# Performance work log

Hardware: AMD Instinct MI355X
Metric: run time of the kernel (lower is better)

Reference implementation:

```python
import jax, jax.numpy as jnp
import numpy as np

BETA = 0.1


def setup_inputs() -> dict:
    key = jax.random.key(0)
    ks = jax.random.split(key, 8)
    B, S, H, V = 4, 512, 2048, 32000
    return {
        "lin_weight": jax.random.normal(ks[0], (V, H), jnp.float32) * 0.02,
        "_input": jax.random.normal(ks[1], (B, S, H), jnp.float32),
        "attention_mask": jnp.ones((B, S), jnp.float32),
        "rewards": jax.random.normal(ks[2], (B,), jnp.float32),
        "bias": jax.random.normal(ks[3], (V,), jnp.float32) * 0.02,
        "ref_input": jax.random.normal(ks[4], (B, S, H), jnp.float32),
        "ref_weight": jax.random.normal(ks[5], (V, H), jnp.float32) * 0.02,
        "ref_bias": jax.random.normal(ks[6], (V,), jnp.float32) * 0.02,
    }


def _seq_logps(x, w, b, mask):
    # logits: [B,S,V]; per-token max log-softmax, masked, summed over seq
    logits = jnp.einsum("bsh,vh->bsv", x, w) + b
    lp = jax.nn.log_softmax(logits, axis=-1)
    seq = (jnp.max(lp, axis=-1) * mask).sum(axis=-1)  # [B]
    return logits, seq


def reference(lin_weight, _input, attention_mask, rewards, bias, ref_input, ref_weight, ref_bias):
    policy_logits, seq_log_probs = _seq_logps(_input, lin_weight, bias, attention_mask)
    _, ref_seq_logps = _seq_logps(ref_input, ref_weight, ref_bias, attention_mask)
    ref_seq_logps = jax.lax.stop_gradient(ref_seq_logps)

    adv = rewards - rewards.mean()
    std = jnp.std(rewards, ddof=1)  # torch unbiased std
    adv = jnp.where(std > 0, adv / std, adv)

    kl_div = seq_log_probs - ref_seq_logps
    loss = (-(adv * seq_log_probs) + BETA * kl_div).mean()

    metrics = (
        seq_log_probs.mean(),
        jnp.std(seq_log_probs, ddof=1),
        policy_logits.mean(),
        kl_div.mean(),
    )
    return (loss,) + metrics
```

## Files before the change

### kernel.cpp

```cpp
#include <hip/hip_runtime.h>
#include <hip/hip_fp16.h>
#include <math.h>

#define TOK 2048
#define HD 2048
#define VOC 32000
#define BM 256
#define BN 256
#define BK 64
#define NT (HD/BK)
#define NCH (VOC/64)
#define NBLK ((TOK/BM)*(VOC/BN))

typedef _Float16 half8 __attribute__((ext_vector_type(8)));
typedef float float4v __attribute__((ext_vector_type(4)));

#define GLB __attribute__((address_space(1)))
#define LDSAS __attribute__((address_space(3)))

static __device__ __forceinline__ void gload_lds16(const void* g, void* l) {
  __builtin_amdgcn_global_load_lds((const GLB unsigned int*)g,
                                   (LDSAS unsigned int*)l, 16, 0, 0);
}

static __device__ __forceinline__ float4v mfma16(half8 a, half8 b, float4v c) {
  return __builtin_amdgcn_mfma_f32_16x16x32_f16(a, b, c, 0, 0, 0);
}

__global__ void cvt_f32_f16(const float* __restrict__ in,
                            _Float16* __restrict__ out, int n8) {
  for (int i = blockIdx.x * blockDim.x + threadIdx.x; i < n8;
       i += gridDim.x * blockDim.x) {
    float4v a = *(const float4v*)(in + (size_t)i*8);
    float4v b = *(const float4v*)(in + (size_t)i*8 + 4);
    half8 h;
    #pragma unroll
    for (int j=0;j<4;j++) { h[j] = (_Float16)a[j]; h[4+j] = (_Float16)b[j]; }
    *(half8*)(out + (size_t)i*8) = h;
  }
}

template<int CB, bool SG1, bool SG2, int VMN>
__device__ __forceinline__ void ktile(
    unsigned char* ldsby, const char* Xb, const char* Wb,
    int sA0, int sA1, int sB0, int sB1, int ldst0, int ldst1, int kbn,
    const int (&aofs)[8], const int (&bofs)[4], float4v (&acc)[8][4])
{
  constexpr int U0 = CB, U1 = CB + 16384, U2 = CB + 32768, U3 = CB + 49152;
  half8 af1[8], bf1[4], af2lo[4], bf2[4], af2hi[4];

  #pragma unroll
  for (int n=0;n<4;n++) bf1[n] = *(const half8*)(ldsby + U1 + bofs[n]);
  #pragma unroll
  for (int m=0;m<8;m++) af1[m] = *(const half8*)(ldsby + U0 + aofs[m]);
  if (SG1) {
    gload_lds16(Xb + (sA0 + kbn + 64), ldsby + ((CB^65536) + 32768) + ldst0);
    gload_lds16(Xb + (sA1 + kbn + 64), ldsby + ((CB^65536) + 32768) + ldst1);
    gload_lds16(Wb + (sB0 + kbn + 64), ldsby + ((CB^65536) + 49152) + ldst0);
    gload_lds16(Wb + (sB1 + kbn + 64), ldsby + ((CB^65536) + 49152) + ldst1);
  }
  __builtin_amdgcn_s_setprio(1);
  #pragma unroll
  for (int m=0;m<4;m++)
    #pragma unroll
    for (int n=0;n<4;n++)
      acc[m][n] = mfma16(af1[m], bf1[n], acc[m][n]);
  #pragma unroll
  for (int n=0;n<4;n++) bf2[n]   = *(const half8*)(ldsby + U3 + bofs[n]);
  #pragma unroll
  for (int m=0;m<4;m++) af2lo[m] = *(const half8*)(ldsby + U2 + aofs[m]);
  #pragma unroll
  for (int m=4;m<8;m++)
    #pragma unroll
    for (int n=0;n<4;n++)
      acc[m][n] = mfma16(af1[m], bf1[n], acc[m][n]);
  __builtin_amdgcn_s_setprio(0);
  __builtin_amdgcn_s_barrier();

  #pragma unroll
  for (int m=0;m<4;m++) af2hi[m] = *(const half8*)(ldsby + U2 + aofs[4+m]);
  if (SG2) {
    gload_lds16(Xb + (sA0 + kbn + 128), ldsby + (CB + 0)     + ldst0);
    gload_lds16(Xb + (sA1 + kbn + 128), ldsby + (CB + 0)     + ldst1);
    gload_lds16(Wb + (sB0 + kbn + 128), ldsby + (CB + 16384) + ldst0);
    gload_lds16(Wb + (sB1 + kbn + 128), ldsby + (CB + 16384) + ldst1);
  }
  __builtin_amdgcn_s_setprio(1);
  #pragma unroll
  for (int m=0;m<4;m++)
    #pragma unroll
    for (int n=0;n<4;n++)
      acc[m][n] = mfma16(af2lo[m], bf2[n], acc[m][n]);
  #pragma unroll
  for (int m=0;m<4;m++)
    #pragma unroll
    for (int n=0;n<4;n++)
      acc[4+m][n] = mfma16(af2hi[m], bf2[n], acc[4+m][n]);
  __builtin_amdgcn_s_setprio(0);
  if (VMN == 4)      asm volatile("s_waitcnt vmcnt(4)" ::: "memory");
  else if (VMN == 0) asm volatile("s_waitcnt vmcnt(0)" ::: "memory");
  __builtin_amdgcn_s_barrier();
}

__global__ __launch_bounds__(512, 2) void gemm_stats_f16(
    const _Float16* __restrict__ Xh, const _Float16* __restrict__ Wh,
    const float* __restrict__ bias,
    float* __restrict__ pmax, float* __restrict__ psum,
    float* __restrict__ bsum, int computeSum)
{
  __shared__ unsigned char ldsbuf[131072];
  unsigned char* ldsby = ldsbuf;

  int bid = blockIdx.x;
  int swz = (bid & 7) * (NBLK/8) + (bid >> 3);
  int rowt = swz & 7;
  int colt = swz >> 3;
  int brow = rowt * BM;
  int bcol = colt * BN;

  int tid  = threadIdx.x;
  int lane = tid & 63;
  int wv   = tid >> 6;
  int wr   = wv >> 2;
  int wc   = wv & 3;
  int l15  = lane & 15;
  int q    = lane >> 4;

  int aswz = (((((l15 & 1) << 2) | q) ^ ((l15 >> 1) & 7)) << 4) + ((l15 >> 1) << 7);
  int aofs[8], bofs[4];
  #pragma unroll
  for (int m = 0; m < 8; m++) aofs[m] = wr*8192 + m*1024 + aswz;
  #pragma unroll
  for (int n = 0; n < 4; n++) bofs[n] = wc*4096 + n*1024 + aswz;

  int s8  = (tid & 7) ^ ((tid >> 3) & 7);
  int rl  = wv*16 + (((tid >> 3) & 7) << 1) + (s8 >> 2);
  int kc  = (s8 & 3) << 4;
  int sA0 = (brow + rl)*(HD*2) + kc;
  int sA1 = sA0 + 128*(HD*2);
  int sB0 = (bcol + rl)*(HD*2) + kc;
  int sB1 = sB0 + 128*(HD*2);
  int ldst0 = (wv << 10);
  int ldst1 = (wv << 10) + 8192;

  const char* Xb = (const char*)Xh;
  const char* Wb = (const char*)Wh;

  float4v acc[8][4];
  #pragma unroll
  for (int m=0;m<8;m++)
    #pragma unroll
    for (int n=0;n<4;n++) acc[m][n] = (float4v){0.f,0.f,0.f,0.f};

  gload_lds16(Xb + sA0,       ldsby + 0     + ldst0);
  gload_lds16(Xb + sA1,       ldsby + 0     + ldst1);
  gload_lds16(Wb + sB0,       ldsby + 16384 + ldst0);
  gload_lds16(Wb + sB1,       ldsby + 16384 + ldst1);
  gload_lds16(Xb + (sA0+64),  ldsby + 32768 + ldst0);
  gload_lds16(Xb + (sA1+64),  ldsby + 32768 + ldst1);
  gload_lds16(Wb + (sB0+64),  ldsby + 49152 + ldst0);
  gload_lds16(Wb + (sB1+64),  ldsby + 49152 + ldst1);
  gload_lds16(Xb + (sA0+128), ldsby + 65536 + ldst0);
  gload_lds16(Xb + (sA1+128), ldsby + 65536 + ldst1);
  gload_lds16(Wb + (sB0+128), ldsby + 81920 + ldst0);
  gload_lds16(Wb + (sB1+128), ldsby + 81920 + ldst1);
  asm volatile("s_waitcnt vmcnt(4)" ::: "memory");
  __builtin_amdgcn_s_barrier();

  int kbn = 128;
  #pragma unroll 1
  for (int i = 0; i < 15; ++i) {
    ktile<0,     true, true, 4>(ldsby, Xb, Wb, sA0,sA1,sB0,sB1, ldst0,ldst1, kbn, aofs, bofs, acc);
    kbn += 128;
    ktile<65536, true, true, 4>(ldsby, Xb, Wb, sA0,sA1,sB0,sB1, ldst0,ldst1, kbn, aofs, bofs, acc);
    kbn += 128;
  }
  ktile<0,     true,  false, 0>(ldsby, Xb, Wb, sA0,sA1,sB0,sB1, ldst0,ldst1, kbn, aofs, bofs, acc);
  kbn += 128;
  ktile<65536, false, false, -1>(ldsby, Xb, Wb, sA0,sA1,sB0,sB1, ldst0,ldst1, kbn, aofs, bofs, acc);

  float bv[4];
  #pragma unroll
  for (int n=0;n<4;n++) bv[n] = bias[bcol + wc*64 + n*16 + l15];

  float lsum = 0.f;
  int ch = colt*4 + wc;
  #pragma unroll
  for (int m=0;m<8;m++) {
    #pragma unroll
    for (int r=0;r<4;r++) {
      float v0 = acc[m][0][r] + bv[0];
      float v1 = acc[m][1][r] + bv[1];
      float v2 = acc[m][2][r] + bv[2];
      float v3 = acc[m][3][r] + bv[3];
      if (computeSum) lsum += v0+v1+v2+v3;
      float mx = fmaxf(fmaxf(v0,v1), fmaxf(v2,v3));
      #pragma unroll
      for (int off=1; off<16; off<<=1) mx = fmaxf(mx, __shfl_xor(mx, off, 64));
      float se = __expf(v0-mx)+__expf(v1-mx)+__expf(v2-mx)+__expf(v3-mx);
      #pragma unroll
      for (int off=1; off<16; off<<=1) se += __shfl_xor(se, off, 64);
      if (l15 == 0) {
        int row = brow + wr*128 + m*16 + (lane>>4)*4 + r;
        pmax[(size_t)row*NCH + ch] = mx;
        psum[(size_t)row*NCH + ch] = se;
      }
    }
  }

  if (computeSum) {
    #pragma unroll
    for (int off=1; off<64; off<<=1) lsum += __shfl_xor(lsum, off, 64);
    __syncthreads();
    float* red = (float*)ldsbuf;
    if (lane == 0) red[wv] = lsum;
    __syncthreads();
    if (tid == 0) {
      float s = 0.f;
      for (int w=0; w<8; w++) s += red[w];
      bsum[blockIdx.x] = s;
    }
  }
}

__global__ void row_combine(const float* __restrict__ pmax,
                            const float* __restrict__ psum,
                            const float* __restrict__ mask,
                            float* __restrict__ tok)
{
  int row = blockIdx.x;
  int lane = threadIdx.x;
  float M = -INFINITY;
  for (int c = lane; c < NCH; c += 64) M = fmaxf(M, pmax[(size_t)row*NCH + c]);
  #pragma unroll
  for (int off=1; off<64; off<<=1) M = fmaxf(M, __shfl_xor(M, off, 64));
  float L = 0.f;
  for (int c = lane; c < NCH; c += 64)
    L += psum[(size_t)row*NCH + c] * __expf(pmax[(size_t)row*NCH + c] - M);
  #pragma unroll
  for (int off=1; off<64; off<<=1) L += __shfl_xor(L, off, 64);
  if (lane == 0) tok[row] = -logf(L) * mask[row];
}

__global__ void finalize(const float* __restrict__ tokP,
                         const float* __restrict__ tokR,
                         const float* __restrict__ rewards,
                         const float* __restrict__ bsum, int nbsum,
                         float* __restrict__ out)
{
  __shared__ float red[256];
  __shared__ float seqP[4], seqR[4];
  int t = threadIdx.x;
  for (int b=0; b<4; b++) {
    float v = tokP[b*512 + t] + tokP[b*512 + 256 + t];
    red[t] = v; __syncthreads();
    for (int s=128; s>0; s>>=1) { if (t < s) red[t] += red[t+s]; __syncthreads(); }
    if (t == 0) seqP[b] = red[0];
    __syncthreads();
    v = tokR[b*512 + t] + tokR[b*512 + 256 + t];
    red[t] = v; __syncthreads();
    for (int s=128; s>0; s>>=1) { if (t < s) red[t] += red[t+s]; __syncthreads(); }
    if (t == 0) seqR[b] = red[0];
    __syncthreads();
  }
  float ls = 0.f;
  for (int i=t; i<nbsum; i+=256) ls += bsum[i];
  red[t] = ls; __syncthreads();
  for (int s=128; s>0; s>>=1) { if (t < s) red[t] += red[t+s]; __syncthreads(); }
  if (t == 0) {
    float r0=rewards[0], r1=rewards[1], r2=rewards[2], r3=rewards[3];
    float rm = (r0+r1+r2+r3)*0.25f;
    float var = ((r0-rm)*(r0-rm)+(r1-rm)*(r1-rm)+(r2-rm)*(r2-rm)+(r3-rm)*(r3-rm))/3.f;
    float rstd = sqrtf(var);
    float adv[4] = {r0-rm, r1-rm, r2-rm, r3-rm};
    if (rstd > 0.f) { for (int b=0;b<4;b++) adv[b] /= rstd; }
    float loss=0.f, sm=0.f, km=0.f;
    for (int b=0;b<4;b++) {
      float kl = seqP[b] - seqR[b];
      loss += -(adv[b]*seqP[b]) + 0.1f*kl;
      sm += seqP[b]; km += kl;
    }
    loss *= 0.25f; sm *= 0.25f; km *= 0.25f;
    float sv = 0.f;
    for (int b=0;b<4;b++) { float d = seqP[b]-sm; sv += d*d; }
    float sstd = sqrtf(sv/3.f);
    out[0] = loss;
    out[1] = sm;
    out[2] = sstd;
    out[3] = red[0] / ((float)TOK * (float)VOC);
    out[4] = km;
  }
}

extern "C" void kernel_launch(void* const* d_in, const int* in_sizes, int n_in,
                              void* d_out, int out_size, void* d_ws, size_t ws_size,
                              hipStream_t stream) {
  const float* W    = (const float*)d_in[0];
  const float* X    = (const float*)d_in[1];
  const float* mask = (const float*)d_in[2];
  const float* rew  = (const float*)d_in[3];
  const float* bias = (const float*)d_in[4];
  const float* Xr   = (const float*)d_in[5];
  const float* Wr   = (const float*)d_in[6];
  const float* br   = (const float*)d_in[7];
  float* out = (float*)d_out;

  float* pmax = (float*)d_ws;
  float* psum = pmax + (size_t)TOK*NCH;
  float* tokP = psum + (size_t)TOK*NCH;
  float* tokR = tokP + TOK;
  float* bsum = tokR + TOK;

  size_t headFloats = (size_t)TOK*NCH*2 + TOK*2 + 4096;
  size_t offXh = headFloats * 4;
  _Float16* Xh = (_Float16*)((unsigned char*)d_ws + offXh);
  _Float16* Wh = (_Float16*)((unsigned char*)d_ws + offXh + (size_t)TOK*HD*2);

  cvt_f32_f16<<<2048, 256, 0, stream>>>(X,  Xh, TOK*HD/8);
  cvt_f32_f16<<<2048, 256, 0, stream>>>(W,  Wh, VOC*HD/8);
  gemm_stats_f16<<<NBLK, 512, 0, stream>>>(Xh, Wh, bias, pmax, psum, bsum, 1);
  row_combine<<<TOK, 64, 0, stream>>>(pmax, psum, mask, tokP);
  cvt_f32_f16<<<2048, 256, 0, stream>>>(Xr, Xh, TOK*HD/8);
  cvt_f32_f16<<<2048, 256, 0, stream>>>(Wr, Wh, VOC*HD/8);
  gemm_stats_f16<<<NBLK, 512, 0, stream>>>(Xh, Wh, br, pmax, psum, bsum, 0);
  row_combine<<<TOK, 64, 0, stream>>>(pmax, psum, mask, tokR);
  finalize<<<1, 256, 0, stream>>>(tokP, tokR, rew, bsum, NBLK, out);
}
```

Measured before the change: 678.5 us.

## Load fp32 weights directly into registers and convert in-kernel, dropping W conversion pass

Removes the separate fp32-to-fp16 conversion kernels for the 32000x2048 weight matrices. The GEMM now reads fp32 W straight from global memory into per-lane registers with a one-step register prefetch, then packs it to fp16 with cvt_pkrtz before the MFMAs. Only the X tile is staged through LDS, so LDS shrinks to 64KB. This removes a full read and write of each weight matrix, but each block reads the weights at twice the bytes from global memory without LDS sharing. It also adds register pressure and uses round-toward-zero conversion.

Result: slower. 1.361 ms (+100.6%).

```diff
diff --git a/kernel.cpp b/kernel.cpp
--- a/kernel.cpp
+++ b/kernel.cpp
@@ -13,6 +13,8 @@
 #define NBLK ((TOK/BM)*(VOC/BN))
 
 typedef _Float16 half8 __attribute__((ext_vector_type(8)));
+typedef _Float16 half2v __attribute__((ext_vector_type(2)));
+typedef __fp16   fp16x2 __attribute__((ext_vector_type(2)));
 typedef float float4v __attribute__((ext_vector_type(4)));
 
 #define GLB __attribute__((address_space(1)))
@@ -25,6 +27,17 @@
 
 static __device__ __forceinline__ float4v mfma16(half8 a, half8 b, float4v c) {
   return __builtin_amdgcn_mfma_f32_16x16x32_f16(a, b, c, 0, 0, 0);
+}
+
+static __device__ __forceinline__ half8 cvt8(float4v a, float4v b) {
+  half2v p0 = __builtin_bit_cast(half2v, __builtin_amdgcn_cvt_pkrtz(a[0], a[1]));
+  half2v p1 = __builtin_bit_cast(half2v, __builtin_amdgcn_cvt_pkrtz(a[2], a[3]));
+  half2v p2 = __builtin_bit_cast(half2v, __builtin_amdgcn_cvt_pkrtz(b[0], b[1]));
+  half2v p3 = __builtin_bit_cast(half2v, __builtin_amdgcn_cvt_pkrtz(b[2], b[3]));
+  half8 h;
+  h[0]=p0[0]; h[1]=p0[1]; h[2]=p1[0]; h[3]=p1[1];
+  h[4]=p2[0]; h[5]=p2[1]; h[6]=p3[0]; h[7]=p3[1];
+  return h;
 }
 
 __global__ void cvt_f32_f16(const float* __restrict__ in,
@@ -40,75 +53,69 @@
   }
 }
 
-template<int CB, bool SG1, bool SG2, int VMN>
+template<int CB, bool SGA1, bool SGA2, bool SGB2>
 __device__ __forceinline__ void ktile(
-    unsigned char* ldsby, const char* Xb, const char* Wb,
-    int sA0, int sA1, int sB0, int sB1, int ldst0, int ldst1, int kbn,
-    const int (&aofs)[8], const int (&bofs)[4], float4v (&acc)[8][4])
+    unsigned char* ldsby, const char* Xb,
+    const char* const (&wb)[4], int koffA,
+    int sA0, int sA1, int ldst0, int ldst1, int kbn,
+    const int (&aofs)[8], float4v (&bstg)[4][2], float4v (&acc)[8][4])
 {
-  constexpr int U0 = CB, U1 = CB + 16384, U2 = CB + 32768, U3 = CB + 49152;
-  half8 af1[8], bf1[4], af2lo[4], bf2[4], af2hi[4];
-
-  #pragma unroll
-  for (int n=0;n<4;n++) bf1[n] = *(const half8*)(ldsby + U1 + bofs[n]);
-  #pragma unroll
-  for (int m=0;m<8;m++) af1[m] = *(const half8*)(ldsby + U0 + aofs[m]);
-  if (SG1) {
-    gload_lds16(Xb + (sA0 + kbn + 64), ldsby + ((CB^65536) + 32768) + ldst0);
-    gload_lds16(Xb + (sA1 + kbn + 64), ldsby + ((CB^65536) + 32768) + ldst1);
-    gload_lds16(Wb + (sB0 + kbn + 64), ldsby + ((CB^65536) + 49152) + ldst0);
-    gload_lds16(Wb + (sB1 + kbn + 64), ldsby + ((CB^65536) + 49152) + ldst1);
+  half8 af[8], bf[4];
+
+  if (SGA1) {
+    gload_lds16(Xb + (sA0 + kbn + 64), ldsby + ((CB^32768) + 16384) + ldst0);
+    gload_lds16(Xb + (sA1 + kbn + 64), ldsby + ((CB^32768) + 16384) + ldst1);
+  }
+  #pragma unroll
+  for (int m=0;m<8;m++) af[m] = *(const half8*)(ldsby + CB + aofs[m]);
+  #pragma unroll
+  for (int n=0;n<4;n++) bf[n] = cvt8(bstg[n][0], bstg[n][1]);
+  #pragma unroll
+  for (int n=0;n<4;n++) {
+    bstg[n][0] = *(const float4v*)(wb[n] + koffA);
+    bstg[n][1] = *(const float4v*)(wb[n] + koffA + 16);
   }
   __builtin_amdgcn_s_setprio(1);
   #pragma unroll
-  for (int m=0;m<4;m++)
+  for (int m=0;m<8;m++)
     #pragma unroll
     for (int n=0;n<4;n++)
-      acc[m][n] = mfma16(af1[m], bf1[n], acc[m][n]);
-  #pragma unroll
-  for (int n=0;n<4;n++) bf2[n]   = *(const half8*)(ldsby + U3 + bofs[n]);
-  #pragma unroll
-  for (int m=0;m<4;m++) af2lo[m] = *(const half8*)(ldsby + U2 + aofs[m]);
-  #pragma unroll
-  for (int m=4;m<8;m++)
-    #pragma unroll
-    for (int n=0;n<4;n++)
-      acc[m][n] = mfma16(af1[m], bf1[n], acc[m][n]);
+      acc[m][n] = mfma16(af[m], bf[n], acc[m][n]);
   __builtin_amdgcn_s_setprio(0);
   __builtin_amdgcn_s_barrier();
 
-  #pragma unroll
-  for (int m=0;m<4;m++) af2hi[m] = *(const half8*)(ldsby + U2 + aofs[4+m]);
-  if (SG2) {
-    gload_lds16(Xb + (sA0 + kbn + 128), ldsby + (CB + 0)     + ldst0);
-    gload_lds16(Xb + (sA1 + kbn + 128), ldsby + (CB + 0)     + ldst1);
-    gload_lds16(Wb + (sB0 + kbn + 128), ldsby + (CB + 16384) + ldst0);
-    gload_lds16(Wb + (sB1 + kbn + 128), ldsby + (CB + 16384) + ldst1);
+  if (SGA2) {
+    gload_lds16(Xb + (sA0 + kbn + 128), ldsby + CB + ldst0);
+    gload_lds16(Xb + (sA1 + kbn + 128), ldsby + CB + ldst1);
+  }
+  #pragma unroll
+  for (int m=0;m<8;m++) af[m] = *(const half8*)(ldsby + CB + 16384 + aofs[m]);
+  #pragma unroll
+  for (int n=0;n<4;n++) bf[n] = cvt8(bstg[n][0], bstg[n][1]);
+  if (SGB2) {
+    #pragma unroll
+    for (int n=0;n<4;n++) {
+      bstg[n][0] = *(const float4v*)(wb[n] + koffA + 128);
+      bstg[n][1] = *(const float4v*)(wb[n] + koffA + 144);
+    }
   }
   __builtin_amdgcn_s_setprio(1);
   #pragma unroll
-  for (int m=0;m<4;m++)
+  for (int m=0;m<8;m++)
     #pragma unroll
     for (int n=0;n<4;n++)
-      acc[m][n] = mfma16(af2lo[m], bf2[n], acc[m][n]);
-  #pragma unroll
-  for (int m=0;m<4;m++)
-    #pragma unroll
-    for (int n=0;n<4;n++)
-      acc[4+m][n] = mfma16(af2hi[m], bf2[n], acc[4+m][n]);
+      acc[m][n] = mfma16(af[m], bf[n], acc[m][n]);
   __builtin_amdgcn_s_setprio(0);
-  if (VMN == 4)      asm volatile("s_waitcnt vmcnt(4)" ::: "memory");
-  else if (VMN == 0) asm volatile("s_waitcnt vmcnt(0)" ::: "memory");
   __builtin_amdgcn_s_barrier();
 }
 
 __global__ __launch_bounds__(512, 2) void gemm_stats_f16(
-    const _Float16* __restrict__ Xh, const _Float16* __restrict__ Wh,
+    const _Float16* __restrict__ Xh, const float* __restrict__ W32,
     const float* __restrict__ bias,
     float* __restrict__ pmax, float* __restrict__ psum,
     float* __restrict__ bsum, int computeSum)
 {
-  __shared__ unsigned char ldsbuf[131072];
+  __shared__ unsigned char ldsbuf[65536];
   unsigned char* ldsby = ldsbuf;
 
   int bid = blockIdx.x;
@@ -127,24 +134,28 @@
   int q    = lane >> 4;
 
   int aswz = (((((l15 & 1) << 2) | q) ^ ((l15 >> 1) & 7)) << 4) + ((l15 >> 1) << 7);
-  int aofs[8], bofs[4];
+  int aofs[8];
   #pragma unroll
   for (int m = 0; m < 8; m++) aofs[m] = wr*8192 + m*1024 + aswz;
-  #pragma unroll
-  for (int n = 0; n < 4; n++) bofs[n] = wc*4096 + n*1024 + aswz;
 
   int s8  = (tid & 7) ^ ((tid >> 3) & 7);
   int rl  = wv*16 + (((tid >> 3) & 7) << 1) + (s8 >> 2);
   int kc  = (s8 & 3) << 4;
   int sA0 = (brow + rl)*(HD*2) + kc;
   int sA1 = sA0 + 128*(HD*2);
-  int sB0 = (bcol + rl)*(HD*2) + kc;
-  int sB1 = sB0 + 128*(HD*2);
   int ldst0 = (wv << 10);
   int ldst1 = (wv << 10) + 8192;
 
   const char* Xb = (const char*)Xh;
-  const char* Wb = (const char*)Wh;
+
+  const char* wb[4];
+  {
+    const char* Wc = (const char*)W32;
+    int v0 = bcol + wc*64 + l15;
+    #pragma unroll
+    for (int n=0;n<4;n++)
+      wb[n] = Wc + (size_t)(v0 + n*16) * (HD*4) + q*32;
+  }
 
   float4v acc[8][4];
   #pragma unroll
@@ -152,32 +163,34 @@
     #pragma unroll
     for (int n=0;n<4;n++) acc[m][n] = (float4v){0.f,0.f,0.f,0.f};
 
+  float4v bstg[4][2];
+
+  #pragma unroll
+  for (int n=0;n<4;n++) {
+    bstg[n][0] = *(const float4v*)(wb[n] + 0);
+    bstg[n][1] = *(const float4v*)(wb[n] + 16);
+  }
   gload_lds16(Xb + sA0,       ldsby + 0     + ldst0);
   gload_lds16(Xb + sA1,       ldsby + 0     + ldst1);
-  gload_lds16(Wb + sB0,       ldsby + 16384 + ldst0);
-  gload_lds16(Wb + sB1,       ldsby + 16384 + ldst1);
-  gload_lds16(Xb + (sA0+64),  ldsby + 32768 + ldst0);
-  gload_lds16(Xb + (sA1+64),  ldsby + 32768 + ldst1);
-  gload_lds16(Wb + (sB0+64),  ldsby + 49152 + ldst0);
-  gload_lds16(Wb + (sB1+64),  ldsby + 49152 + ldst1);
-  gload_lds16(Xb + (sA0+128), ldsby + 65536 + ldst0);
-  gload_lds16(Xb + (sA1+128), ldsby + 65536 + ldst1);
-  gload_lds16(Wb + (sB0+128), ldsby + 81920 + ldst0);
-  gload_lds16(Wb + (sB1+128), ldsby + 81920 + ldst1);
-  asm volatile("s_waitcnt vmcnt(4)" ::: "memory");
+  gload_lds16(Xb + (sA0+64),  ldsby + 16384 + ldst0);
+  gload_lds16(Xb + (sA1+64),  ldsby + 16384 + ldst1);
+  gload_lds16(Xb + (sA0+128), ldsby + 32768 + ldst0);
+  gload_lds16(Xb + (sA1+128), ldsby + 32768 + ldst1);
+  asm volatile("s_waitcnt vmcnt(0)" ::: "memory");
   __builtin_amdgcn_s_barrier();
 
-  int kbn = 128;
+  int kbn   = 128;
+  int koffA = 128;
   #pragma unroll 1
   for (int i = 0; i < 15; ++i) {
-    ktile<0,     true, true, 4>(ldsby, Xb, Wb, sA0,sA1,sB0,sB1, ldst0,ldst1, kbn, aofs, bofs, acc);
-    kbn += 128;
-    ktile<65536, true, true, 4>(ldsby, Xb, Wb, sA0,sA1,sB0,sB1, ldst0,ldst1, kbn, aofs, bofs, acc);
-    kbn += 128;
-  }
-  ktile<0,     true,  false, 0>(ldsby, Xb, Wb, sA0,sA1,sB0,sB1, ldst0,ldst1, kbn, aofs, bofs, acc);
-  kbn += 128;
-  ktile<65536, false, false, -1>(ldsby, Xb, Wb, sA0,sA1,sB0,sB1, ldst0,ldst1, kbn, aofs, bofs, acc);
+    ktile<0,     true, true, true>(ldsby, Xb, wb, koffA, sA0,sA1, ldst0,ldst1, kbn, aofs, bstg, acc);
+    kbn += 128; koffA += 256;
+    ktile<32768, true, true, true>(ldsby, Xb, wb, koffA, sA0,sA1, ldst0,ldst1, kbn, aofs, bstg, acc);
+    kbn += 128; koffA += 256;
+  }
+  ktile<0,     true,  false, true >(ldsby, Xb, wb, koffA, sA0,sA1, ldst0,ldst1, kbn, aofs, bstg, acc);
+  kbn += 128; koffA += 256;
+  ktile<32768, false, false, false>(ldsby, Xb, wb, koffA, sA0,sA1, ldst0,ldst1, kbn, aofs, bstg, acc);
 
   float bv[4];
   #pragma unroll
@@ -314,15 +327,12 @@
   size_t headFloats = (size_t)TOK*NCH*2 + TOK*2 + 4096;
   size_t offXh = headFloats * 4;
   _Float16* Xh = (_Float16*)((unsigned char*)d_ws + offXh);
-  _Float16* Wh = (_Float16*)((unsigned char*)d_ws + offXh + (size_t)TOK*HD*2);
 
   cvt_f32_f16<<<2048, 256, 0, stream>>>(X,  Xh, TOK*HD/8);
-  cvt_f32_f16<<<2048, 256, 0, stream>>>(W,  Wh, VOC*HD/8);
-  gemm_stats_f16<<<NBLK, 512, 0, stream>>>(Xh, Wh, bias, pmax, psum, bsum, 1);
+  gemm_stats_f16<<<NBLK, 512, 0, stream>>>(Xh, W, bias, pmax, psum, bsum, 1);
   row_combine<<<TOK, 64, 0, stream>>>(pmax, psum, mask, tokP);
   cvt_f32_f16<<<2048, 256, 0, stream>>>(Xr, Xh, TOK*HD/8);
-  cvt_f32_f16<<<2048, 256, 0, stream>>>(Wr, Wh, VOC*HD/8);
-  gemm_stats_f16<<<NBLK, 512, 0, stream>>>(Xh, Wh, br, pmax, psum, bsum, 0);
+  gemm_stats_f16<<<NBLK, 512, 0, stream>>>(Xh, Wr, br, pmax, psum, bsum, 0);
   row_combine<<<TOK, 64, 0, stream>>>(pmax, psum, mask, tokR);
   finalize<<<1, 256, 0, stream>>>(tokP, tokR, rew, bsum, NBLK, out);
 }
```

## Prefetch next K-tile LDS fragments across tile boundary in GEMM main loop

Applied to the files above, without the earlier changes.

Restructures the GEMM inner pipeline so the first A/B fragments of the next K-tile are read from LDS during the previous tile's MFMA tail and carried in registers (pfa/pfb). This hides LDS read latency at the start of each tile. A vmcnt wait is added before the mid-tile barrier so the prefetched buffer is ready. The cost is more live VGPRs under a 512x2 launch bound, which risks spills or reduced occupancy, plus an extra wait point that may stall global loads.

After: 679.5 us. Within noise of the previous version (+0.2%).

```diff
diff --git a/kernel.cpp b/kernel.cpp
--- a/kernel.cpp
+++ b/kernel.cpp
@@ -40,19 +40,18 @@
   }
 }
 
-template<int CB, bool SG1, bool SG2, int VMN>
+template<int CB, bool SG1, bool SG2, bool PF, int VM1, int VM2>
 __device__ __forceinline__ void ktile(
     unsigned char* ldsby, const char* Xb, const char* Wb,
-    int sA0, int sA1, int sB0, int sB1, int ldst0, int ldst1, int kbn,
-    const int (&aofs)[8], const int (&bofs)[4], float4v (&acc)[8][4])
+    int sA0, int sA1, int sB0, int sB1,
+    int ldst0, int ldst1, int kbn,
+    const int (&aofs)[8], const int (&bofs)[4],
+    half8 (&pfa)[4], half8 (&pfb)[4], float4v (&acc)[8][4])
 {
-  constexpr int U0 = CB, U1 = CB + 16384, U2 = CB + 32768, U3 = CB + 49152;
-  half8 af1[8], bf1[4], af2lo[4], bf2[4], af2hi[4];
-
-  #pragma unroll
-  for (int n=0;n<4;n++) bf1[n] = *(const half8*)(ldsby + U1 + bofs[n]);
-  #pragma unroll
-  for (int m=0;m<8;m++) af1[m] = *(const half8*)(ldsby + U0 + aofs[m]);
+  half8 hi[4], qalo[4], qb[4];
+
+  #pragma unroll
+  for (int m=0;m<4;m++) hi[m] = *(const half8*)(ldsby + CB + aofs[4+m]);
   if (SG1) {
     gload_lds16(Xb + (sA0 + kbn + 64), ldsby + ((CB^65536) + 32768) + ldst0);
     gload_lds16(Xb + (sA1 + kbn + 64), ldsby + ((CB^65536) + 32768) + ldst1);
@@ -64,24 +63,26 @@
   for (int m=0;m<4;m++)
     #pragma unroll
     for (int n=0;n<4;n++)
-      acc[m][n] = mfma16(af1[m], bf1[n], acc[m][n]);
-  #pragma unroll
-  for (int n=0;n<4;n++) bf2[n]   = *(const half8*)(ldsby + U3 + bofs[n]);
-  #pragma unroll
-  for (int m=0;m<4;m++) af2lo[m] = *(const half8*)(ldsby + U2 + aofs[m]);
-  #pragma unroll
-  for (int m=4;m<8;m++)
+      acc[m][n] = mfma16(pfa[m], pfb[n], acc[m][n]);
+  #pragma unroll
+  for (int n=0;n<4;n++) qb[n]   = *(const half8*)(ldsby + CB + 49152 + bofs[n]);
+  #pragma unroll
+  for (int m=0;m<4;m++) qalo[m] = *(const half8*)(ldsby + CB + 32768 + aofs[m]);
+  #pragma unroll
+  for (int m=0;m<4;m++)
     #pragma unroll
     for (int n=0;n<4;n++)
-      acc[m][n] = mfma16(af1[m], bf1[n], acc[m][n]);
+      acc[4+m][n] = mfma16(hi[m], pfb[n], acc[4+m][n]);
   __builtin_amdgcn_s_setprio(0);
+  if (VM1==4)      asm volatile("s_waitcnt vmcnt(4)" ::: "memory");
+  else if (VM1==0) asm volatile("s_waitcnt vmcnt(0)" ::: "memory");
   __builtin_amdgcn_s_barrier();
 
   #pragma unroll
-  for (int m=0;m<4;m++) af2hi[m] = *(const half8*)(ldsby + U2 + aofs[4+m]);
+  for (int m=0;m<4;m++) hi[m] = *(const half8*)(ldsby + CB + 32768 + aofs[4+m]);
   if (SG2) {
-    gload_lds16(Xb + (sA0 + kbn + 128), ldsby + (CB + 0)     + ldst0);
-    gload_lds16(Xb + (sA1 + kbn + 128), ldsby + (CB + 0)     + ldst1);
+    gload_lds16(Xb + (sA0 + kbn + 128), ldsby + CB + ldst0);
+    gload_lds16(Xb + (sA1 + kbn + 128), ldsby + CB + ldst1);
     gload_lds16(Wb + (sB0 + kbn + 128), ldsby + (CB + 16384) + ldst0);
     gload_lds16(Wb + (sB1 + kbn + 128), ldsby + (CB + 16384) + ldst1);
   }
@@ -90,15 +91,21 @@
   for (int m=0;m<4;m++)
     #pragma unroll
     for (int n=0;n<4;n++)
-      acc[m][n] = mfma16(af2lo[m], bf2[n], acc[m][n]);
+      acc[m][n] = mfma16(qalo[m], qb[n], acc[m][n]);
+  if (PF) {
+    #pragma unroll
+    for (int n=0;n<4;n++) pfb[n] = *(const half8*)(ldsby + (CB^65536) + 16384 + bofs[n]);
+    #pragma unroll
+    for (int m=0;m<4;m++) pfa[m] = *(const half8*)(ldsby + (CB^65536) + aofs[m]);
+  }
   #pragma unroll
   for (int m=0;m<4;m++)
     #pragma unroll
     for (int n=0;n<4;n++)
-      acc[4+m][n] = mfma16(af2hi[m], bf2[n], acc[4+m][n]);
+      acc[4+m][n] = mfma16(hi[m], qb[n], acc[4+m][n]);
   __builtin_amdgcn_s_setprio(0);
-  if (VMN == 4)      asm volatile("s_waitcnt vmcnt(4)" ::: "memory");
-  else if (VMN == 0) asm volatile("s_waitcnt vmcnt(0)" ::: "memory");
+  if (VM2==4)      asm volatile("s_waitcnt vmcnt(4)" ::: "memory");
+  else if (VM2==0) asm volatile("s_waitcnt vmcnt(0)" ::: "memory");
   __builtin_amdgcn_s_barrier();
 }
 
@@ -167,17 +174,23 @@
   asm volatile("s_waitcnt vmcnt(4)" ::: "memory");
   __builtin_amdgcn_s_barrier();
 
+  half8 pfa[4], pfb[4];
+  #pragma unroll
+  for (int n=0;n<4;n++) pfb[n] = *(const half8*)(ldsby + 16384 + bofs[n]);
+  #pragma unroll
+  for (int m=0;m<4;m++) pfa[m] = *(const half8*)(ldsby + aofs[m]);
+
   int kbn = 128;
   #pragma unroll 1
   for (int i = 0; i < 15; ++i) {
-    ktile<0,     true, true, 4>(ldsby, Xb, Wb, sA0,sA1,sB0,sB1, ldst0,ldst1, kbn, aofs, bofs, acc);
+    ktile<0,     true,true,true, 4,4>(ldsby, Xb, Wb, sA0,sA1,sB0,sB1, ldst0,ldst1, kbn, aofs, bofs, pfa, pfb, acc);
     kbn += 128;
-    ktile<65536, true, true, 4>(ldsby, Xb, Wb, sA0,sA1,sB0,sB1, ldst0,ldst1, kbn, aofs, bofs, acc);
+    ktile<65536, true,true,true, 4,4>(ldsby, Xb, Wb, sA0,sA1,sB0,sB1, ldst0,ldst1, kbn, aofs, bofs, pfa, pfb, acc);
     kbn += 128;
   }
-  ktile<0,     true,  false, 0>(ldsby, Xb, Wb, sA0,sA1,sB0,sB1, ldst0,ldst1, kbn, aofs, bofs, acc);
+  ktile<0,     true,false,true, 4,0>(ldsby, Xb, Wb, sA0,sA1,sB0,sB1, ldst0,ldst1, kbn, aofs, bofs, pfa, pfb, acc);
   kbn += 128;
-  ktile<65536, false, false, -1>(ldsby, Xb, Wb, sA0,sA1,sB0,sB1, ldst0,ldst1, kbn, aofs, bofs, acc);
+  ktile<65536, false,false,false, -1,-1>(ldsby, Xb, Wb, sA0,sA1,sB0,sB1, ldst0,ldst1, kbn, aofs, bofs, pfa, pfb, acc);
 
   float bv[4];
   #pragma unroll
```

## Restructure GEMM k-tile into four barrier-separated phases with smaller fragment sets

Applied to the files above, without the earlier changes.

Splits each double k-step into four phases, each loading 4 A and 4 B fragments from LDS and issuing 16 MFMAs. Global-to-LDS prefetches are spread across the phases, and every phase ends with a barrier plus an lgkmcnt wait. This cuts live fragment registers and interleaves loads with compute in a ping-pong style across the two waves per SIMD. The cost is more barriers and sched_barriers, which may serialize work and lose overlap.

Result: no change. 692.0 us (+2.0%).

```diff
diff --git a/kernel.cpp b/kernel.cpp
--- a/kernel.cpp
+++ b/kernel.cpp
@@ -40,62 +40,88 @@
   }
 }
 
-template<int CB, bool SG1, bool SG2, int VMN>
+template<int CB, bool SG01, bool SG23, int VMN>
 __device__ __forceinline__ void ktile(
     unsigned char* ldsby, const char* Xb, const char* Wb,
-    int sA0, int sA1, int sB0, int sB1, int ldst0, int ldst1, int kbn,
+    int sA0, int sA1, int sB0, int sB1,
+    int ldst0, int ldst1, int kbn,
     const int (&aofs)[8], const int (&bofs)[4], float4v (&acc)[8][4])
 {
-  constexpr int U0 = CB, U1 = CB + 16384, U2 = CB + 32768, U3 = CB + 49152;
-  half8 af1[8], bf1[4], af2lo[4], bf2[4], af2hi[4];
-
-  #pragma unroll
-  for (int n=0;n<4;n++) bf1[n] = *(const half8*)(ldsby + U1 + bofs[n]);
-  #pragma unroll
-  for (int m=0;m<8;m++) af1[m] = *(const half8*)(ldsby + U0 + aofs[m]);
-  if (SG1) {
+  half8 af[4], bf[4];
+
+  #pragma unroll
+  for (int m=0;m<4;m++) af[m] = *(const half8*)(ldsby + CB + aofs[m]);
+  #pragma unroll
+  for (int n=0;n<4;n++) bf[n] = *(const half8*)(ldsby + CB + 16384 + bofs[n]);
+  if (SG01) {
     gload_lds16(Xb + (sA0 + kbn + 64), ldsby + ((CB^65536) + 32768) + ldst0);
     gload_lds16(Xb + (sA1 + kbn + 64), ldsby + ((CB^65536) + 32768) + ldst1);
+  }
+  __builtin_amdgcn_s_barrier();
+  asm volatile("s_waitcnt lgkmcnt(0)" ::: "memory");
+  __builtin_amdgcn_sched_barrier(0);
+  __builtin_amdgcn_s_setprio(1);
+  #pragma unroll
+  for (int m=0;m<4;m++)
+    #pragma unroll
+    for (int n=0;n<4;n++)
+      acc[m][n] = mfma16(af[m], bf[n], acc[m][n]);
+  __builtin_amdgcn_s_setprio(0);
+  __builtin_amdgcn_s_barrier();
+
+  #pragma unroll
+  for (int m=0;m<4;m++) af[m] = *(const half8*)(ldsby + CB + aofs[4+m]);
+  if (SG01) {
     gload_lds16(Wb + (sB0 + kbn + 64), ldsby + ((CB^65536) + 49152) + ldst0);
     gload_lds16(Wb + (sB1 + kbn + 64), ldsby + ((CB^65536) + 49152) + ldst1);
   }
+  __builtin_amdgcn_s_barrier();
+  asm volatile("s_waitcnt lgkmcnt(0)" ::: "memory");
+  __builtin_amdgcn_sched_barrier(0);
   __builtin_amdgcn_s_setprio(1);
   #pragma unroll
   for (int m=0;m<4;m++)
     #pragma unroll
     for (int n=0;n<4;n++)
-      acc[m][n] = mfma16(af1[m], bf1[n], acc[m][n]);
-  #pragma unroll
-  for (int n=0;n<4;n++) bf2[n]   = *(const half8*)(ldsby + U3 + bofs[n]);
-  #pragma unroll
-  for (int m=0;m<4;m++) af2lo[m] = *(const half8*)(ldsby + U2 + aofs[m]);
-  #pragma unroll
-  for (int m=4;m<8;m++)
+      acc[4+m][n] = mfma16(af[m], bf[n], acc[4+m][n]);
+  __builtin_amdgcn_s_setprio(0);
+  __builtin_amdgcn_s_barrier();
+
+  #pragma unroll
+  for (int m=0;m<4;m++) af[m] = *(const half8*)(ldsby + CB + 32768 + aofs[m]);
+  #pragma unroll
+  for (int n=0;n<4;n++) bf[n] = *(const half8*)(ldsby + CB + 49152 + bofs[n]);
+  if (SG23) {
+    gload_lds16(Xb + (sA0 + kbn + 128), ldsby + CB + ldst0);
+    gload_lds16(Xb + (sA1 + kbn + 128), ldsby + CB + ldst1);
+  }
+  __builtin_amdgcn_s_barrier();
+  asm volatile("s_waitcnt lgkmcnt(0)" ::: "memory");
+  __builtin_amdgcn_sched_barrier(0);
+  __builtin_amdgcn_s_setprio(1);
+  #pragma unroll
+  for (int m=0;m<4;m++)
     #pragma unroll
     for (int n=0;n<4;n++)
-      acc[m][n] = mfma16(af1[m], bf1[n], acc[m][n]);
+      acc[m][n] = mfma16(af[m], bf[n], acc[m][n]);
   __builtin_amdgcn_s_setprio(0);
   __builtin_amdgcn_s_barrier();
 
   #pragma unroll
-  for (int m=0;m<4;m++) af2hi[m] = *(const half8*)(ldsby + U2 + aofs[4+m]);
-  if (SG2) {
-    gload_lds16(Xb + (sA0 + kbn + 128), ldsby + (CB + 0)     + ldst0);
-    gload_lds16(Xb + (sA1 + kbn + 128), ldsby + (CB + 0)     + ldst1);
+  for (int m=0;m<4;m++) af[m] = *(const half8*)(ldsby + CB + 32768 + aofs[4+m]);
+  if (SG23) {
     gload_lds16(Wb + (sB0 + kbn + 128), ldsby + (CB + 16384) + ldst0);
     gload_lds16(Wb + (sB1 + kbn + 128), ldsby + (CB + 16384) + ldst1);
   }
+  __builtin_amdgcn_s_barrier();
+  asm volatile("s_waitcnt lgkmcnt(0)" ::: "memory");
+  __builtin_amdgcn_sched_barrier(0);
   __builtin_amdgcn_s_setprio(1);
   #pragma unroll
   for (int m=0;m<4;m++)
     #pragma unroll
     for (int n=0;n<4;n++)
-      acc[m][n] = mfma16(af2lo[m], bf2[n], acc[m][n]);
-  #pragma unroll
-  for (int m=0;m<4;m++)
-    #pragma unroll
-    for (int n=0;n<4;n++)
-      acc[4+m][n] = mfma16(af2hi[m], bf2[n], acc[4+m][n]);
+      acc[4+m][n] = mfma16(af[m], bf[n], acc[4+m][n]);
   __builtin_amdgcn_s_setprio(0);
   if (VMN == 4)      asm volatile("s_waitcnt vmcnt(4)" ::: "memory");
   else if (VMN == 0) asm volatile("s_waitcnt vmcnt(0)" ::: "memory");
```
